# Kernel optimization log

Hardware: AMD Instinct MI355X
Metric: run time of the kernel (lower is better)

The kernel has to match this reference:

```python
import jax, jax.numpy as jnp
import numpy as np

B, S, E = 2, 2048, 1024
H = 16
HD = E // H           # 64
KD = 64               # k_dim
VD = 64               # v_dim
SCALE = 1.0 / np.float32(np.sqrt(KD))


def setup_inputs() -> dict:
    key = jax.random.key(0)
    ks = jax.random.split(key, 10)
    return {
        "x": jax.random.normal(ks[0], (B, S, E), dtype=jnp.float32),
        "mask": jax.random.uniform(ks[1], (S, S), dtype=jnp.float32),
        "Wq": jax.random.normal(ks[2], (HD, KD), dtype=jnp.float32) * 0.05,
        "bq": jax.random.normal(ks[3], (KD,), dtype=jnp.float32) * 0.05,
        "Wk": jax.random.normal(ks[4], (HD, KD), dtype=jnp.float32) * 0.05,
        "bk": jax.random.normal(ks[5], (KD,), dtype=jnp.float32) * 0.05,
        "Wv": jax.random.normal(ks[6], (HD, VD), dtype=jnp.float32) * 0.05,
        "bv": jax.random.normal(ks[7], (VD,), dtype=jnp.float32) * 0.05,
        "Wo": jax.random.normal(ks[8], (H * VD, E), dtype=jnp.float32) * 0.05,
        "bo": jax.random.normal(ks[9], (E,), dtype=jnp.float32) * 0.05,
    }


def reference(x, mask, Wq, bq, Wk, bk, Wv, bv, Wo, bo):
    b, s, e = x.shape
    # (B, S, E) -> (B, H, S, head_dim)
    xh = x.reshape(b, s, H, HD).transpose(0, 2, 1, 3)
    q = jnp.einsum('bhsd,dk->bhsk', xh, Wq) + bq   # (B,H,S,KD)
    k = jnp.einsum('bhsd,dk->bhsk', xh, Wk) + bk   # (B,H,S,KD)
    v = jnp.einsum('bhsd,dv->bhsv', xh, Wv) + bv   # (B,H,S,VD)
    sim = jnp.einsum('bhqk,bhsk->bhqs', q, k) * SCALE  # (B,H,S,S)
    sim = sim * mask[None, None, :, :]                  # multiplicative mask
    attn = jax.nn.softmax(sim, axis=-1)
    out = jnp.einsum('bhqs,bhsv->bhqv', attn, v)        # (B,H,S,VD)
    out = out.transpose(0, 2, 1, 3).reshape(b, s, H * VD)
    return out @ Wo + bo
```

## Files before the change

### kernel.cpp

```cpp
#include <hip/hip_runtime.h>
#include <hip/hip_bf16.h>

#define SS 2048
#define EE 1024
#define SCALE 0.125f
#define LOG2E 1.44269504088896f

typedef __attribute__((ext_vector_type(8))) short short8;
typedef __attribute__((ext_vector_type(4))) float float4v;
typedef __attribute__((ext_vector_type(4))) unsigned int uint4v;

__device__ __forceinline__ unsigned short f2bf(float f) {
  unsigned int u = __float_as_uint(f);
  unsigned int lsb = (u >> 16) & 1u;
  u += 0x7fffu + lsb;
  return (unsigned short)(u >> 16);
}
__device__ __forceinline__ unsigned int pk2bf(float a, float b) {
  __hip_bfloat162 h = __float22bfloat162_rn(float2{a, b});
  return *reinterpret_cast<unsigned int*>(&h);
}

__global__ __launch_bounds__(256) void prep_kernel(
    const float* __restrict__ mask,
    const float* __restrict__ Wq, const float* __restrict__ Wk,
    const float* __restrict__ Wv,
    unsigned short* __restrict__ maskP, unsigned short* __restrict__ W3T)
{
  __shared__ unsigned short t[64 * 65];
  int blk = blockIdx.x;
  int tid = threadIdx.x;
  if (blk < 2048) {
    int idx = blk * 256 + tid;
    int lane = idx & 63, step = (idx >> 6) & 63, qt = idx >> 12;
    int li = lane & 15, g = lane >> 4;
    const float c = SCALE * LOG2E;
    const float* mrow = mask + (size_t)(qt * 16 + li) * SS + step * 32 + g * 4;
    float4 a = *(const float4*)mrow;
    float4 bb = *(const float4*)(mrow + 16);
    uint4v o;
    o.x = pk2bf(a.x * c, a.y * c);
    o.y = pk2bf(a.z * c, a.w * c);
    o.z = pk2bf(bb.x * c, bb.y * c);
    o.w = pk2bf(bb.z * c, bb.w * c);
    *(uint4v*)(maskP + (size_t)idx * 8) = o;
    return;
  }
  int m = blk - 2048;
  const float* W = (m == 0) ? Wq : (m == 1 ? Wk : Wv);
#pragma unroll
  for (int i = 0; i < 16; ++i) {
    int e = tid + i * 256; int d = e >> 6, n = e & 63;
    t[n * 65 + d] = f2bf(W[e]);
  }
  __syncthreads();
  unsigned short* dst = W3T + m * 4096;
#pragma unroll
  for (int i = 0; i < 16; ++i) {
    int e = tid + i * 256; int n = e >> 6, d = e & 63;
    dst[n * 64 + d] = t[n * 65 + d];
  }
}

__global__ __launch_bounds__(256) void qkv_kernel(
    const float* __restrict__ x, const unsigned short* __restrict__ W3T,
    const float* __restrict__ bq, const float* __restrict__ bk,
    const float* __restrict__ bv,
    unsigned short* __restrict__ Q, unsigned short* __restrict__ Kp,
    unsigned short* __restrict__ Vf)
{
  __shared__ __align__(16) unsigned short w3t[192 * 72];
  __shared__ __align__(16) unsigned short xt[64 * 72];
  __shared__ __align__(16) unsigned short ob[12288];
  __shared__ float sBias[192];
  int tid = threadIdx.x;
  int bh = blockIdx.x >> 4;
  int s0blk = (blockIdx.x & 15) * 128;
  int b = bh >> 4, h = bh & 15;
  int wv = tid >> 6, lane = tid & 63;
  int li = lane & 15, g = lane >> 4;

#pragma unroll
  for (int i = 0; i < 6; ++i) {
    int slot = tid + i * 256;
    int row = slot >> 3, c = slot & 7;
    *(short8*)(w3t + row * 72 + c * 8) = *(const short8*)(W3T + slot * 8);
  }
  if (tid < 192) sBias[tid] = (tid < 64) ? bq[tid] : (tid < 128 ? bk[tid - 64] : bv[tid - 128]);

  for (int half = 0; half < 2; ++half) {
    int s0 = s0blk + half * 64;
    if (half) __syncthreads();
    const float* xbase = x + ((size_t)(b * SS + s0)) * EE + h * 64;
#pragma unroll
    for (int it = 0; it < 4; ++it) {
      int flat = tid + it * 256;
      int row = flat >> 4, ch = flat & 15;
      float4 v = *(const float4*)(xbase + (size_t)row * EE + ch * 4);
      uint2 u; u.x = pk2bf(v.x, v.y); u.y = pk2bf(v.z, v.w);
      *(uint2*)(xt + row * 72 + ch * 4) = u;
    }
    __syncthreads();

    int mrow = wv * 16;
    short8 af[2];
#pragma unroll
    for (int ks = 0; ks < 2; ++ks)
      af[ks] = *(const short8*)(xt + (mrow + li) * 72 + ks * 32 + g * 8);

    float4v acc[12];
#pragma unroll
    for (int i = 0; i < 12; ++i) acc[i] = (float4v){0, 0, 0, 0};
#pragma unroll
    for (int ks = 0; ks < 2; ++ks)
#pragma unroll
      for (int nb = 0; nb < 12; ++nb) {
        short8 bfr = *(const short8*)(w3t + (nb * 16 + li) * 72 + ks * 32 + g * 8);
        acc[nb] = __builtin_amdgcn_mfma_f32_16x16x32_bf16(af[ks], bfr, acc[nb], 0, 0, 0);
      }

#pragma unroll
    for (int nb = 0; nb < 12; ++nb) {
      float bias = sBias[nb * 16 + li];
      int mtx = nb >> 2, sub = nb & 3;
#pragma unroll
      for (int r = 0; r < 4; ++r) {
        unsigned short v = f2bf(acc[nb][r] + bias);
        int sl = mrow + g * 4 + r;
        int stp = sl >> 5, s5 = sl & 31;
        if (mtx == 0) {
          ob[sl * 64 + sub * 16 + li] = v;
        } else if (mtx == 1) {
          int sb = s5 >> 4, lik = s5 & 15;
          int part = sub >> 1;
          int gk = ((sub & 1) << 1) | (li >> 3);
          ob[4096 + stp * 2048 + (sb * 2 + part) * 512 + (gk * 16 + lik) * 8 + (li & 7)] = v;
        } else {
          int pos = ((s5 >> 2) & 3) * 8 + ((s5 >> 4) & 1) * 4 + (s5 & 3);
          ob[8192 + stp * 2048 + sub * 512 + ((pos >> 3) * 16 + li) * 8 + (pos & 7)] = v;
        }
      }
    }
    __syncthreads();

    unsigned short* Qg = Q + ((size_t)bh * SS + s0) * 64;
    unsigned short* Kg = Kp + (size_t)bh * 131072 + (s0 >> 5) * 2048;
    unsigned short* Vg = Vf + (size_t)bh * 131072 + (s0 >> 5) * 2048;
#pragma unroll
    for (int i = 0; i < 6; ++i) {
      int slot = tid + i * 256;
      int rgn = slot >> 9, off = (slot & 511) * 8;
      short8 v = *(const short8*)(ob + rgn * 4096 + off);
      unsigned short* dst = (rgn == 0) ? (Qg + off) : (rgn == 1 ? (Kg + off) : (Vg + off));
      *(short8*)dst = v;
    }
  }
}

__global__ __launch_bounds__(256) void attn_kernel(
    const unsigned short* __restrict__ Q, const unsigned short* __restrict__ Kp,
    const unsigned short* __restrict__ Vf, const unsigned short* __restrict__ maskP,
    unsigned short* __restrict__ AO)
{
  __shared__ __align__(16) unsigned short tr_all[4 * 32 * 72];
  int tid = threadIdx.x, wv = tid >> 6, lane = tid & 63;
  int li = lane & 15, g = lane >> 4;
  int wave_id = blockIdx.x * 4 + wv;
  int bh = wave_id >> 6;
  int q0 = (wave_id & 63) * 32;

  short8 qf[2][2];
#pragma unroll
  for (int t = 0; t < 2; ++t) {
    const unsigned short* Qb = Q + ((size_t)bh * SS + q0 + t * 16 + li) * 64;
    qf[t][0] = *(const short8*)(Qb + g * 8);
    qf[t][1] = *(const short8*)(Qb + 32 + g * 8);
  }

  const unsigned short* Kg = Kp + (size_t)bh * 131072 + lane * 8;
  const unsigned short* Vg = Vf + (size_t)bh * 131072 + lane * 8;
  const unsigned short* Mg0 = maskP + (size_t)(q0 >> 4) * 32768 + lane * 8;
  const unsigned short* Mg1 = Mg0 + 32768;

  unsigned short ov = (li == 0) ? (unsigned short)0x3F80 : (unsigned short)0;
  short8 vones = {(short)ov, (short)ov, (short)ov, (short)ov,
                  (short)ov, (short)ov, (short)ov, (short)ov};

  float4v acc[2][4];
#pragma unroll
  for (int t = 0; t < 2; ++t)
#pragma unroll
    for (int nb = 0; nb < 4; ++nb) acc[t][nb] = (float4v){0, 0, 0, 0};
  float4v accd[2] = {{0, 0, 0, 0}, {0, 0, 0, 0}};

  short8 kA[4], kB[4], vA[4], vB[4];
  uint4v mA0, mA1, mB0, mB1;
#pragma unroll
  for (int i = 0; i < 4; ++i) {
    kA[i] = *(const short8*)(Kg + i * 512);
    vA[i] = *(const short8*)(Vg + i * 512);
    kB[i] = *(const short8*)(Kg + 2048 + i * 512);
    vB[i] = *(const short8*)(Vg + 2048 + i * 512);
  }
  mA0 = *(const uint4v*)Mg0;
  mA1 = *(const uint4v*)Mg1;
  mB0 = *(const uint4v*)(Mg0 + 512);
  mB1 = *(const uint4v*)(Mg1 + 512);

  auto do_step = [&](short8 (&kf)[4], short8 (&vf)[4], uint4v& m0c, uint4v& m1c,
                     int pfs) {
    short8 pf[2];
#pragma unroll
    for (int t = 0; t < 2; ++t) {
      uint4v pw;
#pragma unroll
      for (int sb = 0; sb < 2; ++sb) {
        float4v st = {0, 0, 0, 0};
        st = __builtin_amdgcn_mfma_f32_16x16x32_bf16(kf[sb * 2], qf[t][0], st, 0, 0, 0);
        st = __builtin_amdgcn_mfma_f32_16x16x32_bf16(kf[sb * 2 + 1], qf[t][1], st, 0, 0, 0);
#pragma unroll
        for (int hh = 0; hh < 2; ++hh) {
          unsigned int mm = (t == 0) ? m0c[sb * 2 + hh] : m1c[sb * 2 + hh];
          float p0 = __builtin_amdgcn_exp2f(st[2 * hh] * __uint_as_float(mm << 16));
          float p1 = __builtin_amdgcn_exp2f(st[2 * hh + 1] * __uint_as_float(mm & 0xffff0000u));
          pw[sb * 2 + hh] = pk2bf(p0, p1);
        }
      }
      pf[t] = *(short8*)&pw;
    }
#pragma unroll
    for (int i = 0; i < 4; ++i)
      kf[i] = *(const short8*)(Kg + (size_t)pfs * 2048 + i * 512);
    m0c = *(const uint4v*)(Mg0 + (size_t)pfs * 512);
    m1c = *(const uint4v*)(Mg1 + (size_t)pfs * 512);
#pragma unroll
    for (int nb = 0; nb < 4; ++nb) {
      acc[0][nb] = __builtin_amdgcn_mfma_f32_16x16x32_bf16(vf[nb], pf[0], acc[0][nb], 0, 0, 0);
      acc[1][nb] = __builtin_amdgcn_mfma_f32_16x16x32_bf16(vf[nb], pf[1], acc[1][nb], 0, 0, 0);
    }
    accd[0] = __builtin_amdgcn_mfma_f32_16x16x32_bf16(vones, pf[0], accd[0], 0, 0, 0);
    accd[1] = __builtin_amdgcn_mfma_f32_16x16x32_bf16(vones, pf[1], accd[1], 0, 0, 0);
#pragma unroll
    for (int i = 0; i < 4; ++i)
      vf[i] = *(const short8*)(Vg + (size_t)pfs * 2048 + i * 512);
  };

  for (int su = 0; su < 32; ++su) {
    do_step(kA, vA, mA0, mA1, (2 * su + 2) & 63);
    do_step(kB, vB, mB0, mB1, (2 * su + 3) & 63);
  }

  unsigned short* tr = tr_all + wv * (32 * 72);
#pragma unroll
  for (int t = 0; t < 2; ++t) {
    float den = __shfl(accd[t][0], li, 64);
    float rd = 1.0f / den;
#pragma unroll
    for (int nb = 0; nb < 4; ++nb) {
      int base = (t * 16 + li) * 72 + nb * 16 + g * 4;
      *(unsigned int*)(tr + base)     = pk2bf(acc[t][nb][0] * rd, acc[t][nb][1] * rd);
      *(unsigned int*)(tr + base + 2) = pk2bf(acc[t][nb][2] * rd, acc[t][nb][3] * rd);
    }
  }
  asm volatile("s_waitcnt lgkmcnt(0)" ::: "memory");

  int b = bh >> 4, h = bh & 15;
  int rrow = lane >> 3, part = lane & 7;
#pragma unroll
  for (int i = 0; i < 4; ++i) {
    int row = i * 8 + rrow;
    short8 o = *(const short8*)(tr + row * 72 + part * 8);
    *(short8*)(AO + ((size_t)(b * SS + q0 + row)) * EE + h * 64 + part * 8) = o;
  }
}

__global__ __launch_bounds__(256) void out_gemm(
    const unsigned short* __restrict__ AO, const float* __restrict__ Wo,
    const float* __restrict__ bo, float* __restrict__ out)
{
  __shared__ __align__(16) unsigned short at[128 * 72];
  __shared__ __align__(16) unsigned short bt[64 * 72];
  int tid = threadIdx.x, wv = tid >> 6, lane = tid & 63;
  int li = lane & 15, g = lane >> 4;
  int m0 = (blockIdx.x >> 4) * 128;
  int n0 = (blockIdx.x & 15) * 64;
  int wm = (wv & 1) * 64, wn = (wv >> 1) * 32;

  const unsigned short* Ag = AO + (size_t)m0 * 1024;
  const float* Bg = Wo + n0;
  int srow = tid >> 3, scol = (tid & 7) * 8;
  int bkrow = tid >> 4, bch = tid & 15;

  short8 apre[4];
  float4 bpre[4];
  auto ldst = [&](int k0) {
#pragma unroll
    for (int i = 0; i < 4; ++i)
      apre[i] = *(const short8*)(Ag + (size_t)(srow + i * 32) * 1024 + k0 + scol);
#pragma unroll
    for (int i = 0; i < 4; ++i)
      bpre[i] = *(const float4*)(Bg + (size_t)(k0 + bkrow + i * 16) * 1024 + bch * 4);
  };

  float4v acc[4][2];
#pragma unroll
  for (int mt = 0; mt < 4; ++mt)
#pragma unroll
    for (int nt = 0; nt < 2; ++nt) acc[mt][nt] = (float4v){0, 0, 0, 0};

  ldst(0);
  for (int k0 = 0; k0 < 1024; k0 += 64) {
    __syncthreads();
#pragma unroll
    for (int i = 0; i < 4; ++i)
      *(short8*)(at + (srow + i * 32) * 72 + scol) = apre[i];
#pragma unroll
    for (int i = 0; i < 4; ++i) {
      int kr = bkrow + i * 16;
      float4 v = bpre[i];
      bt[(bch * 4 + 0) * 72 + kr] = f2bf(v.x);
      bt[(bch * 4 + 1) * 72 + kr] = f2bf(v.y);
      bt[(bch * 4 + 2) * 72 + kr] = f2bf(v.z);
      bt[(bch * 4 + 3) * 72 + kr] = f2bf(v.w);
    }
    int nk = (k0 + 64 < 1024) ? k0 + 64 : 0;
    ldst(nk);
    __syncthreads();
#pragma unroll
    for (int ks = 0; ks < 2; ++ks) {
      short8 afr[4], bfr[2];
#pragma unroll
      for (int mt = 0; mt < 4; ++mt)
        afr[mt] = *(const short8*)(at + (wm + mt * 16 + li) * 72 + ks * 32 + g * 8);
#pragma unroll
      for (int nt = 0; nt < 2; ++nt)
        bfr[nt] = *(const short8*)(bt + (wn + nt * 16 + li) * 72 + ks * 32 + g * 8);
#pragma unroll
      for (int mt = 0; mt < 4; ++mt)
#pragma unroll
        for (int nt = 0; nt < 2; ++nt)
          acc[mt][nt] = __builtin_amdgcn_mfma_f32_16x16x32_bf16(afr[mt], bfr[nt], acc[mt][nt], 0, 0, 0);
    }
  }
#pragma unroll
  for (int nt = 0; nt < 2; ++nt) {
    float bof = bo[n0 + wn + nt * 16 + li];
#pragma unroll
    for (int mt = 0; mt < 4; ++mt)
#pragma unroll
      for (int r = 0; r < 4; ++r)
        out[(size_t)(m0 + wm + mt * 16 + g * 4 + r) * 1024 + n0 + wn + nt * 16 + li] =
            acc[mt][nt][r] + bof;
  }
}

extern "C" void kernel_launch(void* const* d_in, const int* in_sizes, int n_in,
                              void* d_out, int out_size, void* d_ws, size_t ws_size,
                              hipStream_t stream) {
  const float* x    = (const float*)d_in[0];
  const float* mask = (const float*)d_in[1];
  const float* Wq   = (const float*)d_in[2];
  const float* bq   = (const float*)d_in[3];
  const float* Wk   = (const float*)d_in[4];
  const float* bk   = (const float*)d_in[5];
  const float* Wv   = (const float*)d_in[6];
  const float* bv   = (const float*)d_in[7];
  const float* Wo   = (const float*)d_in[8];
  const float* bo   = (const float*)d_in[9];
  float* out = (float*)d_out;

  unsigned short* ws = (unsigned short*)d_ws;
  unsigned short* Q     = ws;
  unsigned short* Kp    = ws + 4194304;
  unsigned short* Vf    = ws + 8388608;
  unsigned short* AO    = ws + 12582912;
  unsigned short* maskP = ws + 16777216;
  unsigned short* W3T = AO;

  prep_kernel<<<2051, 256, 0, stream>>>(mask, Wq, Wk, Wv, maskP, W3T);
  qkv_kernel<<<512, 256, 0, stream>>>(x, W3T, bq, bk, bv, Q, Kp, Vf);
  attn_kernel<<<512, 256, 0, stream>>>(Q, Kp, Vf, maskP, AO);
  out_gemm<<<512, 256, 0, stream>>>(AO, Wo, bo, out);
}
```

Before: 185.0 us.

## Split attention key range across wave pairs and combine partial sums via LDS

```diff
diff --git a/kernel.cpp b/kernel.cpp
--- a/kernel.cpp
+++ b/kernel.cpp
@@ -157,17 +157,23 @@
   }
 }
 
-__global__ __launch_bounds__(256) void attn_kernel(
+__global__ __launch_bounds__(256, 4) void attn_kernel(
     const unsigned short* __restrict__ Q, const unsigned short* __restrict__ Kp,
     const unsigned short* __restrict__ Vf, const unsigned short* __restrict__ maskP,
     unsigned short* __restrict__ AO)
 {
-  __shared__ __align__(16) unsigned short tr_all[4 * 32 * 72];
+  __shared__ __align__(16) float cacc[2][64][36];
+  __shared__ __align__(16) unsigned short tr_all[2][32 * 72];
   int tid = threadIdx.x, wv = tid >> 6, lane = tid & 63;
   int li = lane & 15, g = lane >> 4;
-  int wave_id = blockIdx.x * 4 + wv;
-  int bh = wave_id >> 6;
-  int q0 = (wave_id & 63) * 32;
+  int virt = (blockIdx.x & 7) * 128 + (blockIdx.x >> 3);
+  int wave_id = virt * 4 + wv;
+  int pair = wave_id >> 1;
+  int kh = wave_id & 1;
+  int pw = wv >> 1;
+  int bh = pair >> 6;
+  int q0 = (pair & 63) * 32;
+  int ks0 = kh << 5;
 
   short8 qf[2][2];
 #pragma unroll
@@ -197,22 +203,22 @@
   uint4v mA0, mA1, mB0, mB1;
 #pragma unroll
   for (int i = 0; i < 4; ++i) {
-    kA[i] = *(const short8*)(Kg + i * 512);
-    vA[i] = *(const short8*)(Vg + i * 512);
-    kB[i] = *(const short8*)(Kg + 2048 + i * 512);
-    vB[i] = *(const short8*)(Vg + 2048 + i * 512);
-  }
-  mA0 = *(const uint4v*)Mg0;
-  mA1 = *(const uint4v*)Mg1;
-  mB0 = *(const uint4v*)(Mg0 + 512);
-  mB1 = *(const uint4v*)(Mg1 + 512);
+    kA[i] = *(const short8*)(Kg + (size_t)ks0 * 2048 + i * 512);
+    vA[i] = *(const short8*)(Vg + (size_t)ks0 * 2048 + i * 512);
+    kB[i] = *(const short8*)(Kg + (size_t)(ks0 + 1) * 2048 + i * 512);
+    vB[i] = *(const short8*)(Vg + (size_t)(ks0 + 1) * 2048 + i * 512);
+  }
+  mA0 = *(const uint4v*)(Mg0 + (size_t)ks0 * 512);
+  mA1 = *(const uint4v*)(Mg1 + (size_t)ks0 * 512);
+  mB0 = *(const uint4v*)(Mg0 + (size_t)(ks0 + 1) * 512);
+  mB1 = *(const uint4v*)(Mg1 + (size_t)(ks0 + 1) * 512);
 
   auto do_step = [&](short8 (&kf)[4], short8 (&vf)[4], uint4v& m0c, uint4v& m1c,
                      int pfs) {
     short8 pf[2];
 #pragma unroll
     for (int t = 0; t < 2; ++t) {
-      uint4v pw;
+      uint4v pw2;
 #pragma unroll
       for (int sb = 0; sb < 2; ++sb) {
         float4v st = {0, 0, 0, 0};
@@ -223,10 +229,10 @@
           unsigned int mm = (t == 0) ? m0c[sb * 2 + hh] : m1c[sb * 2 + hh];
           float p0 = __builtin_amdgcn_exp2f(st[2 * hh] * __uint_as_float(mm << 16));
           float p1 = __builtin_amdgcn_exp2f(st[2 * hh + 1] * __uint_as_float(mm & 0xffff0000u));
-          pw[sb * 2 + hh] = pk2bf(p0, p1);
+          pw2[sb * 2 + hh] = pk2bf(p0, p1);
         }
       }
-      pf[t] = *(short8*)&pw;
+      pf[t] = *(short8*)&pw2;
     }
 #pragma unroll
     for (int i = 0; i < 4; ++i)
@@ -245,32 +251,48 @@
       vf[i] = *(const short8*)(Vg + (size_t)pfs * 2048 + i * 512);
   };
 
-  for (int su = 0; su < 32; ++su) {
-    do_step(kA, vA, mA0, mA1, (2 * su + 2) & 63);
-    do_step(kB, vB, mB0, mB1, (2 * su + 3) & 63);
-  }
-
-  unsigned short* tr = tr_all + wv * (32 * 72);
-#pragma unroll
-  for (int t = 0; t < 2; ++t) {
-    float den = __shfl(accd[t][0], li, 64);
-    float rd = 1.0f / den;
-#pragma unroll
-    for (int nb = 0; nb < 4; ++nb) {
-      int base = (t * 16 + li) * 72 + nb * 16 + g * 4;
-      *(unsigned int*)(tr + base)     = pk2bf(acc[t][nb][0] * rd, acc[t][nb][1] * rd);
-      *(unsigned int*)(tr + base + 2) = pk2bf(acc[t][nb][2] * rd, acc[t][nb][3] * rd);
-    }
-  }
-  asm volatile("s_waitcnt lgkmcnt(0)" ::: "memory");
-
-  int b = bh >> 4, h = bh & 15;
-  int rrow = lane >> 3, part = lane & 7;
-#pragma unroll
-  for (int i = 0; i < 4; ++i) {
-    int row = i * 8 + rrow;
-    short8 o = *(const short8*)(tr + row * 72 + part * 8);
-    *(short8*)(AO + ((size_t)(b * SS + q0 + row)) * EE + h * 64 + part * 8) = o;
+  for (int su = 0; su < 16; ++su) {
+    do_step(kA, vA, mA0, mA1, ks0 + ((2 * su + 2) & 31));
+    do_step(kB, vB, mB0, mB1, ks0 + ((2 * su + 3) & 31));
+  }
+
+  if (kh) {
+    float* dst = &cacc[pw][lane][0];
+#pragma unroll
+    for (int t = 0; t < 2; ++t)
+#pragma unroll
+      for (int nb = 0; nb < 4; ++nb)
+        *(float4v*)(dst + t * 16 + nb * 4) = acc[t][nb];
+    dst[32] = accd[0][0];
+    dst[33] = accd[1][0];
+  }
+  __syncthreads();
+  if (kh == 0) {
+    const float* src = &cacc[pw][lane][0];
+    unsigned short* tr = tr_all[pw];
+#pragma unroll
+    for (int t = 0; t < 2; ++t) {
+      float den = __shfl(accd[t][0] + src[32 + t], li, 64);
+      float rd = 1.0f / den;
+#pragma unroll
+      for (int nb = 0; nb < 4; ++nb) {
+        float4v s4 = *(const float4v*)(src + t * 16 + nb * 4);
+        float4v a4 = acc[t][nb];
+        int base = (t * 16 + li) * 72 + nb * 16 + g * 4;
+        *(unsigned int*)(tr + base)     = pk2bf((a4[0] + s4[0]) * rd, (a4[1] + s4[1]) * rd);
+        *(unsigned int*)(tr + base + 2) = pk2bf((a4[2] + s4[2]) * rd, (a4[3] + s4[3]) * rd);
+      }
+    }
+    asm volatile("s_waitcnt lgkmcnt(0)" ::: "memory");
+
+    int b = bh >> 4, h = bh & 15;
+    int rrow = lane >> 3, part = lane & 7;
+#pragma unroll
+    for (int i = 0; i < 4; ++i) {
+      int row = i * 8 + rrow;
+      short8 o = *(const short8*)(tr + row * 72 + part * 8);
+      *(short8*)(AO + ((size_t)(b * SS + q0 + row)) * EE + h * 64 + part * 8) = o;
+    }
   }
 }
 
@@ -379,6 +401,6 @@
 
   prep_kernel<<<2051, 256, 0, stream>>>(mask, Wq, Wk, Wv, maskP, W3T);
   qkv_kernel<<<512, 256, 0, stream>>>(x, W3T, bq, bk, bv, Q, Kp, Vf);
-  attn_kernel<<<512, 256, 0, stream>>>(Q, Kp, Vf, maskP, AO);
+  attn_kernel<<<1024, 256, 0, stream>>>(Q, Kp, Vf, maskP, AO);
   out_gemm<<<512, 256, 0, stream>>>(AO, Wo, bo, out);
 }
```

Measured after the change: 268.4 us. +45.1%, slower.

## Software-pipeline QK^T MFMA one step ahead of softmax and PV

Applied to the files above, without the earlier changes.

```diff
diff --git a/kernel.cpp b/kernel.cpp
--- a/kernel.cpp
+++ b/kernel.cpp
@@ -193,46 +193,67 @@
     for (int nb = 0; nb < 4; ++nb) acc[t][nb] = (float4v){0, 0, 0, 0};
   float4v accd[2] = {{0, 0, 0, 0}, {0, 0, 0, 0}};
 
+  float4v st[2][2];
+
   short8 kA[4], kB[4], vA[4], vB[4];
   uint4v mA0, mA1, mB0, mB1;
-#pragma unroll
-  for (int i = 0; i < 4; ++i) {
-    kA[i] = *(const short8*)(Kg + i * 512);
-    vA[i] = *(const short8*)(Vg + i * 512);
-    kB[i] = *(const short8*)(Kg + 2048 + i * 512);
-    vB[i] = *(const short8*)(Vg + 2048 + i * 512);
-  }
-  mA0 = *(const uint4v*)Mg0;
-  mA1 = *(const uint4v*)Mg1;
-  mB0 = *(const uint4v*)(Mg0 + 512);
-  mB1 = *(const uint4v*)(Mg1 + 512);
-
-  auto do_step = [&](short8 (&kf)[4], short8 (&vf)[4], uint4v& m0c, uint4v& m1c,
-                     int pfs) {
+  {
+    short8 k0[4];
+#pragma unroll
+    for (int i = 0; i < 4; ++i) {
+      k0[i] = *(const short8*)(Kg + i * 512);
+      kA[i] = *(const short8*)(Kg + 2048 + i * 512);
+      kB[i] = *(const short8*)(Kg + 2 * 2048 + i * 512);
+      vA[i] = *(const short8*)(Vg + i * 512);
+      vB[i] = *(const short8*)(Vg + 2048 + i * 512);
+    }
+    mA0 = *(const uint4v*)Mg0;
+    mA1 = *(const uint4v*)Mg1;
+    mB0 = *(const uint4v*)(Mg0 + 512);
+    mB1 = *(const uint4v*)(Mg1 + 512);
+#pragma unroll
+    for (int t = 0; t < 2; ++t)
+#pragma unroll
+      for (int sb = 0; sb < 2; ++sb) {
+        float4v s = {0, 0, 0, 0};
+        s = __builtin_amdgcn_mfma_f32_16x16x32_bf16(k0[sb * 2], qf[t][0], s, 0, 0, 0);
+        s = __builtin_amdgcn_mfma_f32_16x16x32_bf16(k0[sb * 2 + 1], qf[t][1], s, 0, 0, 0);
+        st[t][sb] = s;
+      }
+  }
+
+  auto half_step = [&](short8 (&kf)[4], short8 (&vf)[4], uint4v& m0c, uint4v& m1c,
+                       int kn, int vn, int mn) {
     short8 pf[2];
 #pragma unroll
     for (int t = 0; t < 2; ++t) {
-      uint4v pw;
+      uint4v pw2;
 #pragma unroll
       for (int sb = 0; sb < 2; ++sb) {
-        float4v st = {0, 0, 0, 0};
-        st = __builtin_amdgcn_mfma_f32_16x16x32_bf16(kf[sb * 2], qf[t][0], st, 0, 0, 0);
-        st = __builtin_amdgcn_mfma_f32_16x16x32_bf16(kf[sb * 2 + 1], qf[t][1], st, 0, 0, 0);
 #pragma unroll
         for (int hh = 0; hh < 2; ++hh) {
           unsigned int mm = (t == 0) ? m0c[sb * 2 + hh] : m1c[sb * 2 + hh];
-          float p0 = __builtin_amdgcn_exp2f(st[2 * hh] * __uint_as_float(mm << 16));
-          float p1 = __builtin_amdgcn_exp2f(st[2 * hh + 1] * __uint_as_float(mm & 0xffff0000u));
-          pw[sb * 2 + hh] = pk2bf(p0, p1);
+          float p0 = __builtin_amdgcn_exp2f(st[t][sb][2 * hh] * __uint_as_float(mm << 16));
+          float p1 = __builtin_amdgcn_exp2f(st[t][sb][2 * hh + 1] * __uint_as_float(mm & 0xffff0000u));
+          pw2[sb * 2 + hh] = pk2bf(p0, p1);
         }
       }
-      pf[t] = *(short8*)&pw;
-    }
+      pf[t] = *(short8*)&pw2;
+    }
+    m0c = *(const uint4v*)(Mg0 + (size_t)mn * 512);
+    m1c = *(const uint4v*)(Mg1 + (size_t)mn * 512);
+#pragma unroll
+    for (int t = 0; t < 2; ++t)
+#pragma unroll
+      for (int sb = 0; sb < 2; ++sb) {
+        float4v s = {0, 0, 0, 0};
+        s = __builtin_amdgcn_mfma_f32_16x16x32_bf16(kf[sb * 2], qf[t][0], s, 0, 0, 0);
+        s = __builtin_amdgcn_mfma_f32_16x16x32_bf16(kf[sb * 2 + 1], qf[t][1], s, 0, 0, 0);
+        st[t][sb] = s;
+      }
 #pragma unroll
     for (int i = 0; i < 4; ++i)
-      kf[i] = *(const short8*)(Kg + (size_t)pfs * 2048 + i * 512);
-    m0c = *(const uint4v*)(Mg0 + (size_t)pfs * 512);
-    m1c = *(const uint4v*)(Mg1 + (size_t)pfs * 512);
+      kf[i] = *(const short8*)(Kg + (size_t)kn * 2048 + i * 512);
 #pragma unroll
     for (int nb = 0; nb < 4; ++nb) {
       acc[0][nb] = __builtin_amdgcn_mfma_f32_16x16x32_bf16(vf[nb], pf[0], acc[0][nb], 0, 0, 0);
@@ -242,12 +263,12 @@
     accd[1] = __builtin_amdgcn_mfma_f32_16x16x32_bf16(vones, pf[1], accd[1], 0, 0, 0);
 #pragma unroll
     for (int i = 0; i < 4; ++i)
-      vf[i] = *(const short8*)(Vg + (size_t)pfs * 2048 + i * 512);
+      vf[i] = *(const short8*)(Vg + (size_t)vn * 2048 + i * 512);
   };
 
   for (int su = 0; su < 32; ++su) {
-    do_step(kA, vA, mA0, mA1, (2 * su + 2) & 63);
-    do_step(kB, vB, mB0, mB1, (2 * su + 3) & 63);
+    half_step(kA, vA, mA0, mA1, (2 * su + 3) & 63, (2 * su + 2) & 63, (2 * su + 2) & 63);
+    half_step(kB, vB, mB0, mB1, (2 * su + 4) & 63, (2 * su + 3) & 63, (2 * su + 3) & 63);
   }
 
   unsigned short* tr = tr_all + wv * (32 * 72);
```

After: 191.5 us. 3.6% more time.
